# Performance work log

Measured on AMD Instinct MI355X. Metric: run time of the kernel, lower is better.

## Reference

```python
import jax, jax.numpy as jnp
import numpy as np

V, H, B, S, L = 32000, 512, 256, 128, 5
KAIMING_STD = float(np.sqrt(2.0 / H))  # kaiming_normal_ on (B,H): fan_in=H, gain=sqrt(2)
UNIF = float(1.0 / np.sqrt(H))         # torch LSTMCell/Linear default init scale


def setup_inputs() -> dict:
    key = jax.random.key(0)
    ks = jax.random.split(key, 12)
    x = jax.random.randint(ks[0], (B, S), 0, V)
    h0 = jax.random.normal(ks[1], (L, B, H), jnp.float32) * KAIMING_STD
    c0 = jax.random.normal(ks[2], (L, B, H), jnp.float32) * KAIMING_STD
    emb = jax.random.normal(ks[3], (V, H), jnp.float32)
    emb = emb.at[0].set(0.0)  # padding_idx=0
    W_ih = jax.random.uniform(ks[4], (L, 4 * H, H), jnp.float32, -UNIF, UNIF)
    W_hh = jax.random.uniform(ks[5], (L, 4 * H, H), jnp.float32, -UNIF, UNIF)
    b_ih = jax.random.uniform(ks[6], (L, 4 * H), jnp.float32, -UNIF, UNIF)
    b_hh = jax.random.uniform(ks[7], (L, 4 * H), jnp.float32, -UNIF, UNIF)
    W_out = jax.random.uniform(ks[8], (V, H), jnp.float32, -UNIF, UNIF)
    b_out = jax.random.uniform(ks[9], (V,), jnp.float32, -UNIF, UNIF)
    return {"x": x, "h0": h0, "c0": c0, "emb": emb, "W_ih": W_ih, "W_hh": W_hh,
            "b_ih": b_ih, "b_hh": b_hh, "W_out": W_out, "b_out": b_out}


def reference(x, h0, c0, emb, W_ih, W_hh, b_ih, b_hh, W_out, b_out):
    e = emb[x]                      # (B, S, H)
    seq = e.reshape(S, B, H)        # faithful replica of torch .view(S, B, -1) memory reinterpretation

    def step(carry, xt):
        h, c = carry                # each (L, B, H)
        inp = xt
        hs, cs = [], []
        for l in range(L):
            gates = inp @ W_ih[l].T + b_ih[l] + h[l] @ W_hh[l].T + b_hh[l]  # (B, 4H)
            i, f, g, o = jnp.split(gates, 4, axis=-1)
            i = jax.nn.sigmoid(i)
            f = jax.nn.sigmoid(f)
            g = jnp.tanh(g)
            o = jax.nn.sigmoid(o)
            cn = f * c[l] + i * g
            hn = o * jnp.tanh(cn)
            hs.append(hn)
            cs.append(cn)
            inp = hn
        return (jnp.stack(hs), jnp.stack(cs)), None

    (h, c), _ = jax.lax.scan(step, (h0, c0), seq)
    return h[L - 1] @ W_out.T + b_out  # (B, V)
```

## Files before the change

kernel.cpp:

```cpp
#include <hip/hip_runtime.h>
#include <hip/hip_bf16.h>

#define VOCAB 32000
#define HID 512
#define BATCH 256
#define SEQ 128
#define NL 5
#define BH (BATCH*HID)
#define G4H (4*HID)
#define NBLK 160

typedef __attribute__((ext_vector_type(8))) short short8;
typedef __attribute__((ext_vector_type(4))) float float4v;
typedef __attribute__((ext_vector_type(4))) unsigned int uint4v;

__device__ __forceinline__ float sigmoid_f(float x) {
    return 1.f / (1.f + __expf(-x));
}
__device__ __forceinline__ float tanh_f(float x) {
    float ax = fabsf(x);
    float e = __expf(2.f * ax);
    float t = 1.f - 2.f / (e + 1.f);
    return copysignf(t, x);
}
__device__ __forceinline__ short bf16bits(float f) {
    union { __hip_bfloat16 b; short s; } u;
    u.b = __float2bfloat16(f);
    return u.s;
}
__device__ __forceinline__ short8 load8f(const float* p) {
    float4v lo = *(const float4v*)p;
    float4v hi = *(const float4v*)(p + 4);
    short8 r;
    r[0] = bf16bits(lo[0]); r[1] = bf16bits(lo[1]);
    r[2] = bf16bits(lo[2]); r[3] = bf16bits(lo[3]);
    r[4] = bf16bits(hi[0]); r[5] = bf16bits(hi[1]);
    r[6] = bf16bits(hi[2]); r[7] = bf16bits(hi[3]);
    return r;
}
__device__ __forceinline__ short8 load8b(const __hip_bfloat16* p) {
    return *(const short8*)p;
}

#if __has_builtin(__builtin_amdgcn_make_buffer_rsrc) && \
    __has_builtin(__builtin_amdgcn_raw_buffer_load_b128) && \
    __has_builtin(__builtin_amdgcn_raw_buffer_store_b128)
typedef __amdgpu_buffer_rsrc_t srd_t;
__device__ __forceinline__ srd_t make_srd(const void* p) {
    return __builtin_amdgcn_make_buffer_rsrc(const_cast<void*>(p), (short)0,
                                             0xFFFFFFFFu, 0x00020000);
}
__device__ __forceinline__ short8 bload16(srd_t srd, int voff, int soff) {
    union { uint4v u; short8 s; } c;
    c.u = __builtin_amdgcn_raw_buffer_load_b128(srd, voff, soff, 17);
    return c.s;
}
__device__ __forceinline__ void bstore16(short8 v, srd_t srd, int voff) {
    union { uint4v u; short8 s; } c; c.s = v;
    __builtin_amdgcn_raw_buffer_store_b128(c.u, srd, voff, 0, 17);
}
#else
typedef const char* srd_t;
__device__ __forceinline__ srd_t make_srd(const void* p) {
    return (const char*)p;
}
__device__ __forceinline__ short8 bload16(srd_t srd, int voff, int soff) {
    const char* base = srd + voff + soff;
    union { unsigned long long q[2]; short8 s; } u;
    u.q[0] = __hip_atomic_load((const unsigned long long*)base,
                               __ATOMIC_RELAXED, __HIP_MEMORY_SCOPE_AGENT);
    u.q[1] = __hip_atomic_load((const unsigned long long*)(base + 8),
                               __ATOMIC_RELAXED, __HIP_MEMORY_SCOPE_AGENT);
    return u.s;
}
__device__ __forceinline__ void bstore16(short8 v, srd_t srd, int voff) {
    char* base = const_cast<char*>(srd) + voff;
    union { unsigned long long q[2]; short8 s; } u; u.s = v;
    __hip_atomic_store((unsigned long long*)base, u.q[0],
                       __ATOMIC_RELAXED, __HIP_MEMORY_SCOPE_AGENT);
    __hip_atomic_store((unsigned long long*)(base + 8), u.q[1],
                       __ATOMIC_RELAXED, __HIP_MEMORY_SCOPE_AGENT);
}
#endif

__host__ __device__ constexpr size_t hidx(int s, int l, int j, int m, int c) {
    return ((((size_t)s * NL + l) * 32 + j) * 256 + m) * 16 + c;
}

template<int BIGWS>
__device__ __forceinline__ short8 hload(const __hip_bfloat16* hbuf, srd_t srd,
                                        size_t off, int d) {
    if constexpr (BIGWS) {
        return *(const short8*)((const char*)hbuf + off + (size_t)d * 16384);
    } else {
        return bload16(srd, (int)off, d * 16384);
    }
}

__global__ void init_state_k(const float* __restrict__ h0,
                             __hip_bfloat16* __restrict__ hbuf,
                             int* __restrict__ done, int islot) {
    int i = blockIdx.x * 256 + threadIdx.x;
    int l = i / BH, r = i % BH;
    int m = r >> 9, col = r & 511;
    hbuf[hidx(islot, l, col >> 4, m, col & 15)] = __float2bfloat16(h0[i]);
    if (blockIdx.x == 0 && threadIdx.x < NL) done[threadIdx.x * 64] = 0;
}

template<int BIGWS>
__global__ __launch_bounds__(1024) void lstm_persist_k(
    const int* __restrict__ x,
    const float* __restrict__ emb,
    const float* __restrict__ W_ih,
    const float* __restrict__ W_hh,
    const float* __restrict__ b_ih,
    const float* __restrict__ b_hh,
    const float* __restrict__ c0,
    __hip_bfloat16* __restrict__ hbuf,
    int* __restrict__ done)
{
    __shared__ short lw[65536];
    __shared__ short8 xch[16][32];

    const int tid = threadIdx.x;
    const int xcd = blockIdx.x & 7;
    const int ixc = blockIdx.x >> 3;
    const int slot = xcd * 20 + ixc;
    const int l = slot >> 5;
    const int j = slot & 31;
    const int jbase = j << 4;

    const int wave = tid >> 6, lane = tid & 63;
    const int quad = lane >> 4, l16 = lane & 15;
    const int m16 = wave << 4;

    const float* Wg[2] = { W_ih + (size_t)l * G4H * HID,
                           W_hh + (size_t)l * G4H * HID };

    for (int e = tid; e < 8192; e += 1024) {
        int row = e >> 6;
        int kc  = (e & 63) << 3;
        int gemm = row >> 6, r2 = row & 63, g = r2 >> 4, rl = r2 & 15;
        const float* src = Wg[gemm] + (size_t)(g * HID + jbase + rl) * HID + kc;
        short8 v = load8f(src);
        int kt = kc >> 5, q = (kc >> 3) & 3;
        int fragslot = ((gemm * 4 + g) * 16 + kt) * 64 + (q * 16 + rl);
        *(short8*)&lw[(size_t)fragslot * 8] = v;
    }

    const int jj = jbase + l16;
    float bias[4], c_r[4];
#pragma unroll
    for (int g = 0; g < 4; ++g)
        bias[g] = b_ih[l * G4H + g * HID + jj] + b_hh[l * G4H + g * HID + jj];
#pragma unroll
    for (int r = 0; r < 4; ++r)
        c_r[r] = c0[(size_t)l * BH + (size_t)(m16 + quad * 4 + r) * HID + jj];

    const short* lwb = lw + (size_t)lane * 8;
    const int shi = quad >> 1;
    const size_t abyte = (size_t)(((m16 + l16) * 16 + (quad & 1) * 8) * 2)
                       + (size_t)shi * 8192;
    const srd_t hsrd = make_srd(hbuf);

    __syncthreads();

    for (int t = 0; t < SEQ; ++t) {
        if (tid == 0) {
            if (l > 0) {
                int need = 32 * (t + 1);
                while (__hip_atomic_load(&done[(l - 1) * 64], __ATOMIC_RELAXED,
                                         __HIP_MEMORY_SCOPE_AGENT) < need)
                    __builtin_amdgcn_s_sleep(1);
            }
            if (t > 0) {
                int need = 32 * t;
                while (__hip_atomic_load(&done[l * 64], __ATOMIC_RELAXED,
                                         __HIP_MEMORY_SCOPE_AGENT) < need)
                    __builtin_amdgcn_s_sleep(1);
            }
            if constexpr (!BIGWS) {
                if (l < NL - 1 && t >= 2) {
                    int need = 32 * (t - 1);
                    while (__hip_atomic_load(&done[(l + 1) * 64], __ATOMIC_RELAXED,
                                             __HIP_MEMORY_SCOPE_AGENT) < need)
                        __builtin_amdgcn_s_sleep(1);
                }
            }
        }
        __syncthreads();

        const int p = t & 1, pm1 = p ^ 1;
        const int rslot_prev = BIGWS ? t : pm1;
        const int rslot_in   = BIGWS ? (t + 1) : p;
        const int wslot      = BIGWS ? (t + 1) : p;

        const size_t vpr = 2 * hidx(rslot_prev, l, 0, 0, 0) + abyte;

        float4v acc[4];
#pragma unroll
        for (int g = 0; g < 4; ++g) acc[g] = (float4v){0.f, 0.f, 0.f, 0.f};

        if (l == 0) {
            int tok = x[t * BATCH + m16 + l16];
            const float* ar = emb + (size_t)tok * HID;
            short8 ah[4];
#pragma unroll
            for (int d = 0; d < 4; ++d)
                ah[d] = hload<BIGWS>(hbuf, hsrd, vpr, d);
#pragma unroll
            for (int kt = 0; kt < 16; ++kt) {
                short8 a_in = load8f(ar + kt * 32 + quad * 8);
                short8 a_h = ah[kt & 3];
                if (kt + 4 < 16)
                    ah[kt & 3] = hload<BIGWS>(hbuf, hsrd, vpr, kt + 4);
#pragma unroll
                for (int g = 0; g < 4; ++g) {
                    short8 b0 = *(const short8*)(lwb + (size_t)(g * 16 + kt) * 512);
                    short8 b1 = *(const short8*)(lwb + (size_t)((4 + g) * 16 + kt) * 512);
                    acc[g] = __builtin_amdgcn_mfma_f32_16x16x32_bf16(a_in, b0, acc[g], 0, 0, 0);
                    acc[g] = __builtin_amdgcn_mfma_f32_16x16x32_bf16(a_h,  b1, acc[g], 0, 0, 0);
                }
            }
        } else {
            const size_t vin = 2 * hidx(rslot_in, l - 1, 0, 0, 0) + abyte;
            short8 ai[4], ah[4];
#pragma unroll
            for (int d = 0; d < 4; ++d) {
                ai[d] = hload<BIGWS>(hbuf, hsrd, vin, d);
                ah[d] = hload<BIGWS>(hbuf, hsrd, vpr, d);
            }
#pragma unroll
            for (int kt = 0; kt < 16; ++kt) {
                short8 a_in = ai[kt & 3];
                short8 a_h  = ah[kt & 3];
                if (kt + 4 < 16) {
                    ai[kt & 3] = hload<BIGWS>(hbuf, hsrd, vin, kt + 4);
                    ah[kt & 3] = hload<BIGWS>(hbuf, hsrd, vpr, kt + 4);
                }
#pragma unroll
                for (int g = 0; g < 4; ++g) {
                    short8 b0 = *(const short8*)(lwb + (size_t)(g * 16 + kt) * 512);
                    short8 b1 = *(const short8*)(lwb + (size_t)((4 + g) * 16 + kt) * 512);
                    acc[g] = __builtin_amdgcn_mfma_f32_16x16x32_bf16(a_in, b0, acc[g], 0, 0, 0);
                    acc[g] = __builtin_amdgcn_mfma_f32_16x16x32_bf16(a_h,  b1, acc[g], 0, 0, 0);
                }
            }
        }

        short* xp = (short*)&xch[wave];
#pragma unroll
        for (int r = 0; r < 4; ++r) {
            float iv = sigmoid_f(acc[0][r] + bias[0]);
            float fv = sigmoid_f(acc[1][r] + bias[1]);
            float gv = tanh_f(acc[2][r] + bias[2]);
            float ov = sigmoid_f(acc[3][r] + bias[3]);
            c_r[r] = fv * c_r[r] + iv * gv;
            xp[(quad * 4 + r) * 16 + l16] = bf16bits(ov * tanh_f(c_r[r]));
        }
        __builtin_amdgcn_wave_barrier();
        if (lane < 32) {
            short8 v = *(const short8*)&xp[lane * 8];
            int vout = (int)(2 * hidx(wslot, l, j, m16, 0)) + lane * 16;
            bstore16(v, hsrd, vout);
        }

        __syncthreads();
        if (tid == 0)
            __hip_atomic_fetch_add(&done[l * 64], 1, __ATOMIC_RELEASE,
                                   __HIP_MEMORY_SCOPE_AGENT);
    }
}

__global__ __launch_bounds__(512) void out_gemm_k(
    const __hip_bfloat16* __restrict__ hfin,
    const float* __restrict__ W_out,
    const float* __restrict__ b_out,
    float* __restrict__ out)
{
    const int nb = blockIdx.x;
    const int tid = threadIdx.x;
    const int wave = tid >> 6, lane = tid & 63;
    const int quad = lane >> 4, l16 = lane & 15;
    const int nt = wave & 3, mh = wave >> 2;

    const int shi = quad >> 1;
    const size_t coff = (size_t)(quad & 1) * 8;

    const int ncol = nb * 64 + nt * 16 + l16;
    const float* brow = W_out + (size_t)ncol * HID;

    float4v acc[8];
#pragma unroll
    for (int mt = 0; mt < 8; ++mt) acc[mt] = (float4v){0.f, 0.f, 0.f, 0.f};

#pragma unroll 2
    for (int kt = 0; kt < 16; ++kt) {
        short8 b = load8f(brow + kt * 32 + quad * 8);
        const __hip_bfloat16* abase =
            hfin + (size_t)(2 * kt + shi) * 4096 + coff;
#pragma unroll
        for (int mt = 0; mt < 8; ++mt) {
            short8 a = load8b(abase + (size_t)(mh * 128 + mt * 16 + l16) * 16);
            acc[mt] = __builtin_amdgcn_mfma_f32_16x16x32_bf16(a, b, acc[mt], 0, 0, 0);
        }
    }

    float bo = b_out[ncol];
#pragma unroll
    for (int mt = 0; mt < 8; ++mt) {
#pragma unroll
        for (int r = 0; r < 4; ++r) {
            int m = mh * 128 + mt * 16 + quad * 4 + r;
            out[(size_t)m * VOCAB + ncol] = acc[mt][r] + bo;
        }
    }
}

extern "C" void kernel_launch(void* const* d_in, const int* in_sizes, int n_in,
                              void* d_out, int out_size, void* d_ws, size_t ws_size,
                              hipStream_t stream) {
    const int* x        = (const int*)d_in[0];
    const float* h0     = (const float*)d_in[1];
    const float* c0     = (const float*)d_in[2];
    const float* emb    = (const float*)d_in[3];
    const float* W_ih   = (const float*)d_in[4];
    const float* W_hh   = (const float*)d_in[5];
    const float* b_ih   = (const float*)d_in[6];
    const float* b_hh   = (const float*)d_in[7];
    const float* W_out  = (const float*)d_in[8];
    const float* b_out  = (const float*)d_in[9];
    float* out          = (float*)d_out;

    __hip_bfloat16* hbuf = (__hip_bfloat16*)d_ws;

    const size_t hbytes_big = (size_t)(SEQ + 1) * NL * BH * sizeof(__hip_bfloat16);
    const bool big = ws_size >= hbytes_big + 4096;

    if (big) {
        int* done = (int*)((char*)d_ws + hbytes_big);
        init_state_k<<<(NL * BH) / 256, 256, 0, stream>>>(h0, hbuf, done, 0);
        lstm_persist_k<1><<<NBLK, 1024, 0, stream>>>(x, emb, W_ih, W_hh, b_ih,
                                                     b_hh, c0, hbuf, done);
        out_gemm_k<<<VOCAB / 64, 512, 0, stream>>>(
            hbuf + hidx(SEQ, NL - 1, 0, 0, 0), W_out, b_out, out);
    } else {
        int* done = (int*)((char*)d_ws + (size_t)2 * NL * BH * sizeof(__hip_bfloat16));
        init_state_k<<<(NL * BH) / 256, 256, 0, stream>>>(h0, hbuf, done, 1);
        lstm_persist_k<0><<<NBLK, 1024, 0, stream>>>(x, emb, W_ih, W_hh, b_ih,
                                                     b_hh, c0, hbuf, done);
        out_gemm_k<<<VOCAB / 64, 512, 0, stream>>>(
            hbuf + hidx(1, NL - 1, 0, 0, 0), W_out, b_out, out);
    }
}
```

Measured before the change: 3.014 ms.

## Use a ring buffer of hidden-state slots sized to available workspace

Replaces the all-timesteps hidden-state buffer (or the two-slot fallback) with a ring of as many slots as the workspace holds, capped at SEQ+1. Producer layers wait on the next layer only when the ring would wrap, which lets layers run further ahead of each other than the two-slot scheme allows. The aim is to keep the wavefront pipeline across layers when the workspace is too small for the full history, while reducing the memory footprint. It adds an acquire fence and 32-bit offset arithmetic, and keeps plain vector loads for the ring mode.

```diff
diff --git a/kernel.cpp b/kernel.cpp
--- a/kernel.cpp
+++ b/kernel.cpp
@@ -9,6 +9,9 @@
 #define BH (BATCH*HID)
 #define G4H (4*HID)
 #define NBLK 160
+
+#define LAYB  (32*256*16*2)
+#define SLOTB (NL*LAYB)
 
 typedef __attribute__((ext_vector_type(8))) short short8;
 typedef __attribute__((ext_vector_type(4))) float float4v;
@@ -87,16 +90,6 @@
     return ((((size_t)s * NL + l) * 32 + j) * 256 + m) * 16 + c;
 }
 
-template<int BIGWS>
-__device__ __forceinline__ short8 hload(const __hip_bfloat16* hbuf, srd_t srd,
-                                        size_t off, int d) {
-    if constexpr (BIGWS) {
-        return *(const short8*)((const char*)hbuf + off + (size_t)d * 16384);
-    } else {
-        return bload16(srd, (int)off, d * 16384);
-    }
-}
-
 __global__ void init_state_k(const float* __restrict__ h0,
                              __hip_bfloat16* __restrict__ hbuf,
                              int* __restrict__ done, int islot) {
@@ -107,7 +100,7 @@
     if (blockIdx.x == 0 && threadIdx.x < NL) done[threadIdx.x * 64] = 0;
 }
 
-template<int BIGWS>
+template<int MODE>
 __global__ __launch_bounds__(1024) void lstm_persist_k(
     const int* __restrict__ x,
     const float* __restrict__ emb,
@@ -117,7 +110,8 @@
     const float* __restrict__ b_hh,
     const float* __restrict__ c0,
     __hip_bfloat16* __restrict__ hbuf,
-    int* __restrict__ done)
+    int* __restrict__ done,
+    int nslot)
 {
     __shared__ short lw[65536];
     __shared__ short8 xch[16][32];
@@ -159,11 +153,13 @@
 
     const short* lwb = lw + (size_t)lane * 8;
     const int shi = quad >> 1;
-    const size_t abyte = (size_t)(((m16 + l16) * 16 + (quad & 1) * 8) * 2)
-                       + (size_t)shi * 8192;
+    const int abyte = ((m16 + l16) * 16 + (quad & 1) * 8) * 2 + shi * 8192;
     const srd_t hsrd = make_srd(hbuf);
+    const char* hb = (const char*)hbuf;
 
     __syncthreads();
+
+    int cs = 0, ns = 1;
 
     for (int t = 0; t < SEQ; ++t) {
         if (tid == 0) {
@@ -179,23 +175,31 @@
                                          __HIP_MEMORY_SCOPE_AGENT) < need)
                     __builtin_amdgcn_s_sleep(1);
             }
-            if constexpr (!BIGWS) {
+            if constexpr (MODE == 0) {
                 if (l < NL - 1 && t >= 2) {
                     int need = 32 * (t - 1);
                     while (__hip_atomic_load(&done[(l + 1) * 64], __ATOMIC_RELAXED,
                                              __HIP_MEMORY_SCOPE_AGENT) < need)
                         __builtin_amdgcn_s_sleep(1);
                 }
+            } else {
+                if (l < NL - 1 && t >= nslot) {
+                    int need = 32 * (t - nslot + 1);
+                    while (__hip_atomic_load(&done[(l + 1) * 64], __ATOMIC_RELAXED,
+                                             __HIP_MEMORY_SCOPE_AGENT) < need)
+                        __builtin_amdgcn_s_sleep(1);
+                }
+                __builtin_amdgcn_fence(__ATOMIC_ACQUIRE, "agent");
             }
         }
         __syncthreads();
 
         const int p = t & 1, pm1 = p ^ 1;
-        const int rslot_prev = BIGWS ? t : pm1;
-        const int rslot_in   = BIGWS ? (t + 1) : p;
-        const int wslot      = BIGWS ? (t + 1) : p;
-
-        const size_t vpr = 2 * hidx(rslot_prev, l, 0, 0, 0) + abyte;
+        const int rs_prev = (MODE == 0) ? pm1 : cs;
+        const int rs_in   = (MODE == 0) ? p   : ns;
+        const int ws_     = (MODE == 0) ? p   : ns;
+
+        const int vpr = rs_prev * SLOTB + l * LAYB + abyte;
 
         float4v acc[4];
 #pragma unroll
@@ -207,13 +211,16 @@
             short8 ah[4];
 #pragma unroll
             for (int d = 0; d < 4; ++d)
-                ah[d] = hload<BIGWS>(hbuf, hsrd, vpr, d);
+                ah[d] = (MODE == 0) ? bload16(hsrd, vpr, d * 16384)
+                                    : *(const short8*)(hb + vpr + d * 16384);
 #pragma unroll
             for (int kt = 0; kt < 16; ++kt) {
                 short8 a_in = load8f(ar + kt * 32 + quad * 8);
                 short8 a_h = ah[kt & 3];
                 if (kt + 4 < 16)
-                    ah[kt & 3] = hload<BIGWS>(hbuf, hsrd, vpr, kt + 4);
+                    ah[kt & 3] = (MODE == 0)
+                        ? bload16(hsrd, vpr, (kt + 4) * 16384)
+                        : *(const short8*)(hb + vpr + (kt + 4) * 16384);
 #pragma unroll
                 for (int g = 0; g < 4; ++g) {
                     short8 b0 = *(const short8*)(lwb + (size_t)(g * 16 + kt) * 512);
@@ -223,20 +230,30 @@
                 }
             }
         } else {
-            const size_t vin = 2 * hidx(rslot_in, l - 1, 0, 0, 0) + abyte;
+            const int vin = rs_in * SLOTB + (l - 1) * LAYB + abyte;
             short8 ai[4], ah[4];
 #pragma unroll
             for (int d = 0; d < 4; ++d) {
-                ai[d] = hload<BIGWS>(hbuf, hsrd, vin, d);
-                ah[d] = hload<BIGWS>(hbuf, hsrd, vpr, d);
+                if constexpr (MODE == 0) {
+                    ai[d] = bload16(hsrd, vin, d * 16384);
+                    ah[d] = bload16(hsrd, vpr, d * 16384);
+                } else {
+                    ai[d] = *(const short8*)(hb + vin + d * 16384);
+                    ah[d] = *(const short8*)(hb + vpr + d * 16384);
+                }
             }
 #pragma unroll
             for (int kt = 0; kt < 16; ++kt) {
                 short8 a_in = ai[kt & 3];
                 short8 a_h  = ah[kt & 3];
                 if (kt + 4 < 16) {
-                    ai[kt & 3] = hload<BIGWS>(hbuf, hsrd, vin, kt + 4);
-                    ah[kt & 3] = hload<BIGWS>(hbuf, hsrd, vpr, kt + 4);
+                    if constexpr (MODE == 0) {
+                        ai[kt & 3] = bload16(hsrd, vin, (kt + 4) * 16384);
+                        ah[kt & 3] = bload16(hsrd, vpr, (kt + 4) * 16384);
+                    } else {
+                        ai[kt & 3] = *(const short8*)(hb + vin + (kt + 4) * 16384);
+                        ah[kt & 3] = *(const short8*)(hb + vpr + (kt + 4) * 16384);
+                    }
                 }
 #pragma unroll
                 for (int g = 0; g < 4; ++g) {
@@ -261,7 +278,7 @@
         __builtin_amdgcn_wave_barrier();
         if (lane < 32) {
             short8 v = *(const short8*)&xp[lane * 8];
-            int vout = (int)(2 * hidx(wslot, l, j, m16, 0)) + lane * 16;
+            int vout = ws_ * SLOTB + l * LAYB + j * 8192 + m16 * 32 + lane * 16;
             bstore16(v, hsrd, vout);
         }
 
@@ -269,6 +286,11 @@
         if (tid == 0)
             __hip_atomic_fetch_add(&done[l * 64], 1, __ATOMIC_RELEASE,
                                    __HIP_MEMORY_SCOPE_AGENT);
+
+        if constexpr (MODE == 1) {
+            cs = ns;
+            ns = (ns + 1 == nslot) ? 0 : ns + 1;
+        }
     }
 }
 
@@ -334,21 +356,22 @@
 
     __hip_bfloat16* hbuf = (__hip_bfloat16*)d_ws;
 
-    const size_t hbytes_big = (size_t)(SEQ + 1) * NL * BH * sizeof(__hip_bfloat16);
-    const bool big = ws_size >= hbytes_big + 4096;
-
-    if (big) {
-        int* done = (int*)((char*)d_ws + hbytes_big);
+    size_t avail = ws_size > 4096 ? ws_size - 4096 : 0;
+    int nslot = (int)(avail / (size_t)SLOTB);
+    if (nslot > SEQ + 1) nslot = SEQ + 1;
+
+    if (nslot >= 3) {
+        int* done = (int*)((char*)d_ws + (size_t)nslot * SLOTB);
         init_state_k<<<(NL * BH) / 256, 256, 0, stream>>>(h0, hbuf, done, 0);
         lstm_persist_k<1><<<NBLK, 1024, 0, stream>>>(x, emb, W_ih, W_hh, b_ih,
-                                                     b_hh, c0, hbuf, done);
+                                                     b_hh, c0, hbuf, done, nslot);
         out_gemm_k<<<VOCAB / 64, 512, 0, stream>>>(
-            hbuf + hidx(SEQ, NL - 1, 0, 0, 0), W_out, b_out, out);
+            hbuf + hidx(SEQ % nslot, NL - 1, 0, 0, 0), W_out, b_out, out);
     } else {
-        int* done = (int*)((char*)d_ws + (size_t)2 * NL * BH * sizeof(__hip_bfloat16));
+        int* done = (int*)((char*)d_ws + (size_t)2 * SLOTB);
         init_state_k<<<(NL * BH) / 256, 256, 0, stream>>>(h0, hbuf, done, 1);
         lstm_persist_k<0><<<NBLK, 1024, 0, stream>>>(x, emb, W_ih, W_hh, b_ih,
-                                                     b_hh, c0, hbuf, done);
+                                                     b_hh, c0, hbuf, done, 2);
         out_gemm_k<<<VOCAB / 64, 512, 0, stream>>>(
             hbuf + hidx(1, NL - 1, 0, 0, 0), W_out, b_out, out);
     }
```

After: 3.148 ms. 1.04x slower.
